# Kernel tuning notes

Measured on AMD Instinct MI355X. Metric: run time of the kernel, lower is better.

## Reference

```python
import jax, jax.numpy as jnp
import numpy as np

B, L, E, H = 64, 512, 128, 256
NEG_INF = -1e9  # finite stand-in for torch's -inf mask fill (same softmax result)


def setup_inputs() -> dict:
    key = jax.random.key(0)
    ks = jax.random.split(key, 12)
    s = 0.02
    return {
        "embed_input": jax.random.normal(ks[0], (B, L, E), jnp.float32),
        "decoder_input": jax.random.normal(ks[1], (B, E), jnp.float32),
        "h0": jax.random.normal(ks[2], (B, H), jnp.float32),
        "c0": jax.random.normal(ks[3], (B, H), jnp.float32),
        "context": jax.random.normal(ks[4], (B, L, H), jnp.float32),
        "Wih": jax.random.normal(ks[5], (E, 4 * H), jnp.float32) * s,
        "bih": jnp.zeros((4 * H,), jnp.float32),
        "Whh": jax.random.normal(ks[6], (H, 4 * H), jnp.float32) * s,
        "bhh": jnp.zeros((4 * H,), jnp.float32),
        "Wo": jax.random.normal(ks[7], (2 * H, H), jnp.float32) * s,
        "bo": jnp.zeros((H,), jnp.float32),
        "Wq": jax.random.normal(ks[8], (H, H), jnp.float32) * s,
        "bq": jnp.zeros((H,), jnp.float32),
        "Wc": jax.random.normal(ks[9], (H, H), jnp.float32) * s,
        "bc": jnp.zeros((H,), jnp.float32),
        "V": jax.random.uniform(ks[10], (H,), jnp.float32, minval=-1.0, maxval=1.0),
    }


def _forward(embed_input, decoder_input, h0, c0, context,
             Wih, bih, Whh, bhh, Wo, bo, Wq, bq, Wc, bc, V):
    Bq, Lq = embed_input.shape[0], embed_input.shape[1]
    # context_linear is a 1x1 conv -> loop-invariant linear; hoist out of the loop
    ctx = context @ Wc + bc  # (B, L, H)
    runner = jnp.arange(Lq)

    def step(carry, _):
        h, c, mask, x = carry
        # fused LSTM gates
        gates = x @ Wih + bih + h @ Whh + bhh  # (B, 4H)
        i_g, f_g, g_g, o_g = jnp.split(gates, 4, axis=1)
        c_t = jax.nn.sigmoid(f_g) * c + jax.nn.sigmoid(i_g) * jnp.tanh(g_g)
        h_t = jax.nn.sigmoid(o_g) * jnp.tanh(c_t)
        # pointer attention (additive, tanh, V-scored)
        q = h_t @ Wq + bq  # (B, H)
        att = jnp.einsum('h,blh->bl', V, jnp.tanh(q[:, None, :] + ctx))  # (B, L)
        att = jnp.where(mask == 0, NEG_INF, att)
        alpha = jax.nn.softmax(att, axis=1)  # (B, L)
        attn_h = jnp.einsum('bl,blh->bh', alpha, ctx)
        h_new = jnp.tanh(jnp.concatenate([attn_h, h_t], axis=1) @ Wo + bo)
        # masked argmax selection + gather of next decoder input
        masked = alpha * mask
        idx = jnp.argmax(masked, axis=1)  # (B,)
        one_hot = (runner[None, :] == idx[:, None]).astype(alpha.dtype)
        mask_new = mask * (1.0 - one_hot)
        x_new = jnp.einsum('bl,bld->bd', one_hot, embed_input)  # (B, E)
        return (h_new, c_t, mask_new, x_new), (alpha, idx)

    mask0 = jnp.ones((Bq, Lq), embed_input.dtype)
    (h_f, c_f, _, _), (alphas, idxs) = jax.lax.scan(
        step, (h0, c0, mask0, decoder_input), None, length=Lq)
    outputs = jnp.transpose(alphas, (1, 2, 0))  # (B, L, T) matching permute(1,2,0)
    pointers = jnp.transpose(idxs, (1, 0))      # (B, T)
    return outputs, pointers, h_f, c_f


def reference(embed_input, decoder_input, h0, c0, context,
              Wih, bih, Whh, bhh, Wo, bo, Wq, bq, Wc, bc, V):
    return _forward(embed_input, decoder_input, h0, c0, context,
                    Wih, bih, Whh, bhh, Wo, bo, Wq, bq, Wc, bc, V)
```

## Files before the change

### kernel.cpp

```cpp
#include <hip/hip_runtime.h>
#include <cstdint>
#include <cstddef>


#define DEV static __device__ __forceinline__

DEV float rl(float v, int l) {
    return __int_as_float(__builtin_amdgcn_readlane(__float_as_int(v), l));
}
DEV float fast_rcp(float d) {
    float r = __builtin_amdgcn_rcpf(d);
    return r * (2.0f - d * r);
}
DEV float fast_tanh(float x) {
    float e = __expf(fminf(2.0f * x, 88.0f));
    return 1.0f - 2.0f * fast_rcp(1.0f + e);
}
DEV float fast_sigmoid(float x) {
    float e = __expf(fminf(-x, 88.0f));
    return fast_rcp(1.0f + e);
}
DEV void st_rel_u32(uint32_t* p, uint32_t v) {
    __hip_atomic_store(p, v, __ATOMIC_RELEASE, __HIP_MEMORY_SCOPE_AGENT);
}
DEV uint32_t ld_acq_u32(const uint32_t* p) {
    return __hip_atomic_load(p, __ATOMIC_ACQUIRE, __HIP_MEMORY_SCOPE_AGENT);
}
DEV void st_f(float* p, float v) {
    __hip_atomic_store(p, v, __ATOMIC_RELAXED, __HIP_MEMORY_SCOPE_AGENT);
}
DEV float ld_f(const float* p) {
    return __hip_atomic_load(p, __ATOMIC_RELAXED, __HIP_MEMORY_SCOPE_AGENT);
}

__global__ __launch_bounds__(256) void k_ctx(const float* __restrict__ cin,
                                             const float* __restrict__ Wc,
                                             const float* __restrict__ bc,
                                             float* __restrict__ cout_) {
    __shared__ float rows[8][256];
    const int tid = threadIdx.x, lane = tid & 63;
    const long bl0 = (long)blockIdx.x * 8;
    for (int i = tid; i < 8 * 256; i += 256)
        rows[i >> 8][i & 255] = cin[bl0 * 256 + i];
    __syncthreads();
    float rr[8][4];
#pragma unroll
    for (int r = 0; r < 8; ++r)
#pragma unroll
        for (int q = 0; q < 4; ++q) rr[r][q] = rows[r][q * 64 + lane];
    float acc[8] = {0, 0, 0, 0, 0, 0, 0, 0};
#pragma unroll
    for (int kq = 0; kq < 4; ++kq) {
        for (int kk = 0; kk < 64; ++kk) {
            float wc = Wc[(kq * 64 + kk) * 256 + tid];
#pragma unroll
            for (int r = 0; r < 8; ++r) acc[r] += rl(rr[r][kq], kk) * wc;
        }
    }
    float bcv = bc[tid];
#pragma unroll
    for (int r = 0; r < 8; ++r) cout_[(bl0 + r) * 256 + tid] = acc[r] + bcv;
}

__global__ __launch_bounds__(256) void k_proj(const float* __restrict__ xin,
                                              const float* __restrict__ Wih,
                                              float* __restrict__ yout) {
    __shared__ float rows[8][128];
    const int tid = threadIdx.x, lane = tid & 63;
    const long bl0 = (long)blockIdx.x * 8;
    for (int i = tid; i < 8 * 128; i += 256)
        rows[i >> 7][i & 127] = xin[bl0 * 128 + i];
    __syncthreads();
    float rr[8][2];
#pragma unroll
    for (int r = 0; r < 8; ++r)
#pragma unroll
        for (int q = 0; q < 2; ++q) rr[r][q] = rows[r][q * 64 + lane];
    float4 acc[8];
#pragma unroll
    for (int r = 0; r < 8; ++r) acc[r] = make_float4(0.f, 0.f, 0.f, 0.f);
#pragma unroll
    for (int eq = 0; eq < 2; ++eq) {
        for (int ee = 0; ee < 64; ++ee) {
            const float4 w4 =
                *(const float4*)(Wih + (size_t)(eq * 64 + ee) * 1024 + tid * 4);
#pragma unroll
            for (int r = 0; r < 8; ++r) {
                float xe = rl(rr[r][eq], ee);
                acc[r].x += xe * w4.x; acc[r].y += xe * w4.y;
                acc[r].z += xe * w4.z; acc[r].w += xe * w4.w;
            }
        }
    }
#pragma unroll
    for (int r = 0; r < 8; ++r)
        *(float4*)(yout + (bl0 + r) * 1024 + tid * 4) = acc[r];
}

__global__ __launch_bounds__(256) void k_tr(const float* __restrict__ aws,
                                            float* __restrict__ out0) {
    __shared__ float tile[32][33];
    const int b = blockIdx.z, l0 = blockIdx.x * 32, t0 = blockIdx.y * 32;
    const int tx = threadIdx.x, ty = threadIdx.y;
    const float* src = aws + ((size_t)b << 18);
    float* dst = out0 + ((size_t)b << 18);
#pragma unroll
    for (int i = 0; i < 32; i += 8)
        tile[ty + i][tx] = src[(size_t)(t0 + ty + i) * 512 + l0 + tx];
    __syncthreads();
#pragma unroll
    for (int i = 0; i < 32; i += 8)
        dst[(size_t)(l0 + ty + i) * 512 + t0 + tx] = tile[tx][ty + i];
}

__global__ __launch_bounds__(1024) void k_zero(uint32_t* fl) {
    fl[threadIdx.x] = 0u;
    fl[1024 + threadIdx.x] = 0u;
}

__global__ __launch_bounds__(1024) void k_main4(
    const float* __restrict__ h0, const float* __restrict__ c0,
    const float* __restrict__ Whh, const float* __restrict__ Wq,
    const float* __restrict__ Wo, const float* __restrict__ bih,
    const float* __restrict__ bhh, const float* __restrict__ bq,
    const float* __restrict__ bo, const float* __restrict__ V,
    const float* __restrict__ ctx_ws, const float* __restrict__ emb_ws,
    const float* __restrict__ dec_ws, float* __restrict__ alpha_ws,
    float* __restrict__ out1, float* __restrict__ out2,
    float* __restrict__ out3, float* cg_ws, float* ca_ws, uint32_t* fl_ws) {
    const int g = blockIdx.x & 63;
    const int q = blockIdx.x >> 6;
    const int tid = threadIdx.x;
    const int lane = tid & 63;
    const int w = tid >> 6;

    __shared__ __align__(16) float h_s[256];
    __shared__ __align__(16) float c_s[256];
    __shared__ __align__(16) float q_s[256];
    __shared__ __align__(16) float ah_s[256];
    __shared__ __align__(16) float bsum_s[1024];
    __shared__ __align__(16) float att_s[512];
    __shared__ __align__(16) float alpha_s[512];
    __shared__ __align__(16) float mask_s[512];
    __shared__ __align__(16) float bq_s[256];
    __shared__ __align__(16) float bo_s[256];
    __shared__ __align__(16) float xp_s[1024];
    __shared__ __align__(16) float red_s[4096];
    __shared__ float wm_s[8], wS_s[8];
    __shared__ int wi_s[8];

    bsum_s[tid] = bih[tid] + bhh[tid];
    if (tid < 256) {
        h_s[tid] = h0[(g << 8) + tid];
        c_s[tid] = c0[(g << 8) + tid];
        bq_s[tid] = bq[tid];
        bo_s[tid] = bo[tid];
        *(float4*)(xp_s + (tid << 2)) =
            *(const float4*)(dec_ws + ((size_t)g << 10) + (tid << 2));
    }
    if (tid < 512) mask_s[tid] = 1.0f;
    const float4 V4 = *(const float4*)(V + (lane << 2));
    const float* cbase = ctx_ws + (((size_t)g << 9) << 8);
    __syncthreads();

    for (int t = 0; t < 512; ++t) {
        const int par = t & 1;
        const size_t gq4 = (size_t)(par * 64 + g) * 4;
        float* cgb = cg_ws + (gq4 << 10);
        float* cab = ca_ws + (gq4 << 7);
        uint32_t* fg = fl_ws + par * 256 + (g << 2);
        uint32_t* fa = fl_ws + 512 + par * 256 + (g << 2);

        if (tid < 256) {
            float hv = h_s[(q << 6) + lane];
            float4 acc = make_float4(0.f, 0.f, 0.f, 0.f);
            const float* wp = Whh + (size_t)(q << 6) * 1024 + (tid << 2);
#pragma unroll 16
            for (int kk = 0; kk < 64; ++kk) {
                float hk = rl(hv, kk);
                const float4 w4 = *(const float4*)(wp + (size_t)kk * 1024);
                acc.x += hk * w4.x; acc.y += hk * w4.y;
                acc.z += hk * w4.z; acc.w += hk * w4.w;
            }
            *(float4*)(red_s + (q << 10) + (tid << 2)) = acc;
        }
        __syncthreads();
        st_f(cgb + (q << 10) + tid, red_s[(q << 10) + tid]);
        __syncthreads();
        if (tid == 0) st_rel_u32(fg + q, (uint32_t)(t + 1));
        if (tid < 3) {
            const int pm = tid + (tid >= q ? 1 : 0);
            while (ld_acq_u32(fg + pm) < (uint32_t)(t + 1))
                __builtin_amdgcn_s_sleep(1);
        }
        __syncthreads();
#pragma unroll
        for (int jj = 0; jj < 4; ++jj)
            if (jj != q) red_s[(jj << 10) + tid] = ld_f(cgb + (jj << 10) + tid);
        __syncthreads();
        if (tid < 256) {
            float gi = red_s[tid] + red_s[1024 + tid] + red_s[2048 + tid] +
                       red_s[3072 + tid] + bsum_s[tid];
            float gf = red_s[256 + tid] + red_s[1280 + tid] +
                       red_s[2304 + tid] + red_s[3328 + tid] +
                       bsum_s[256 + tid];
            float gg = red_s[512 + tid] + red_s[1536 + tid] +
                       red_s[2560 + tid] + red_s[3584 + tid] +
                       bsum_s[512 + tid];
            float go = red_s[768 + tid] + red_s[1792 + tid] +
                       red_s[2816 + tid] + red_s[3840 + tid] +
                       bsum_s[768 + tid];
            gi += xp_s[tid]; gf += xp_s[256 + tid];
            gg += xp_s[512 + tid]; go += xp_s[768 + tid];
            float ig = fast_sigmoid(gi);
            float fg2 = fast_sigmoid(gf);
            float ggt = fast_tanh(gg);
            float og = fast_sigmoid(go);
            float cn = fg2 * c_s[tid] + ig * ggt;
            c_s[tid] = cn;
            h_s[tid] = og * fast_tanh(cn);
        }
        __syncthreads();
        if (tid < 256) {
            const int u = lane;
            const int pq = tid >> 6;
            float hv = h_s[(pq << 6) + u];
            float4 acc = make_float4(0.f, 0.f, 0.f, 0.f);
            const float* wp = Wq + (size_t)(pq << 6) * 256 + (u << 2);
#pragma unroll 8
            for (int kk = 0; kk < 64; ++kk) {
                float hk = rl(hv, kk);
                const float4 w4 = *(const float4*)(wp + (size_t)kk * 256);
                acc.x += hk * w4.x; acc.y += hk * w4.y;
                acc.z += hk * w4.z; acc.w += hk * w4.w;
            }
            *(float4*)(red_s + (pq << 8) + (u << 2)) = acc;
        }
        __syncthreads();
        if (tid < 256)
            q_s[tid] = red_s[tid] + red_s[256 + tid] + red_s[512 + tid] +
                       red_s[768 + tid] + bq_s[tid];
        __syncthreads();
        {
            const float4 q4 = *(const float4*)(q_s + (lane << 2));
#pragma unroll 2
            for (int i = 0; i < 8; ++i) {
                const int l = (q << 7) + (i << 4) + w;
                if (mask_s[l] == 0.f) {
                    if (lane == 0) att_s[l] = -1e9f;
                } else {
                    const float4 cc =
                        *(const float4*)(cbase + ((size_t)l << 8) + (lane << 2));
                    float s = V4.x * fast_tanh(q4.x + cc.x) +
                              V4.y * fast_tanh(q4.y + cc.y) +
                              V4.z * fast_tanh(q4.z + cc.z) +
                              V4.w * fast_tanh(q4.w + cc.w);
#pragma unroll
                    for (int off = 32; off > 0; off >>= 1)
                        s += __shfl_xor(s, off, 64);
                    if (lane == 0) att_s[l] = s;
                }
            }
        }
        __syncthreads();
        if (tid < 128) st_f(cab + (q << 7) + tid, att_s[(q << 7) + tid]);
        __syncthreads();
        if (tid == 0) st_rel_u32(fa + q, (uint32_t)(t + 1));
        if (tid < 3) {
            const int pm = tid + (tid >= q ? 1 : 0);
            while (ld_acq_u32(fa + pm) < (uint32_t)(t + 1))
                __builtin_amdgcn_s_sleep(1);
        }
        __syncthreads();
        if (tid < 384) {
            const int rel = tid >> 7;
            const int pm = rel + (rel >= q ? 1 : 0);
            const int word = tid & 127;
            att_s[(pm << 7) + word] = ld_f(cab + (pm << 7) + word);
        }
        __syncthreads();
        if (tid < 512) {
            float v = att_s[tid];
            int bi = tid;
#pragma unroll
            for (int off = 1; off < 64; off <<= 1) {
                float ov = __shfl_xor(v, off, 64);
                int oi = __shfl_xor(bi, off, 64);
                if (ov > v || (ov == v && oi < bi)) { v = ov; bi = oi; }
            }
            if (lane == 0) { wm_s[w] = v; wi_s[w] = bi; }
        }
        __syncthreads();
        float e_r = 0.f;
        float m_r; int idx_r;
        {
            m_r = wm_s[0]; idx_r = wi_s[0];
#pragma unroll
            for (int i = 1; i < 8; ++i) {
                float v2 = wm_s[i]; int i2 = wi_s[i];
                if (v2 > m_r || (v2 == m_r && i2 < idx_r)) { m_r = v2; idx_r = i2; }
            }
            if (tid < 512) {
                e_r = __expf(att_s[tid] - m_r);
                float ss = e_r;
#pragma unroll
                for (int off = 32; off > 0; off >>= 1)
                    ss += __shfl_xor(ss, off, 64);
                if (lane == 0) wS_s[w] = ss;
            }
        }
        __syncthreads();
        {
            float S = 0.f;
#pragma unroll
            for (int i = 0; i < 8; ++i) S += wS_s[i];
            if (tid < 512) {
                float a = e_r / S;
                alpha_s[tid] = a;
                if ((tid >> 7) == q)
                    alpha_ws[((((size_t)g << 9) + t) << 9) + tid] = a;
            }
            if (q == 0 && tid == 0) out1[(g << 9) + t] = (float)idx_r;
            if (tid == 0) mask_s[idx_r] = 0.f;
            if (tid < 256)
                *(float4*)(xp_s + (tid << 2)) = *(const float4*)(
                    emb_ws + ((size_t)((g << 9) + idx_r) << 10) + (tid << 2));
        }
        __syncthreads();
        {
            float ax = 0.f, ay = 0.f, az = 0.f, aw = 0.f;
            const float* cb2 = cbase + (lane << 2);
            for (int l = w; l < 512; l += 16) {
                float al = alpha_s[l];
                if (al != 0.f) {
                    const float4 cc = *(const float4*)(cb2 + ((size_t)l << 8));
                    ax += al * cc.x; ay += al * cc.y;
                    az += al * cc.z; aw += al * cc.w;
                }
            }
            *(float4*)(red_s + (w << 8) + (lane << 2)) =
                make_float4(ax, ay, az, aw);
        }
        __syncthreads();
        if (tid < 256) {
            float s = 0.f;
#pragma unroll
            for (int i = 0; i < 16; ++i) s += red_s[(i << 8) + tid];
            ah_s[tid] = s;
        }
        __syncthreads();
        if (tid < 256) {
            const int pq = tid >> 6;
            const float* src0 = (pq < 2) ? ah_s : h_s;
            float av0 = src0[((pq & 1) << 7) + lane];
            float av1 = src0[((pq & 1) << 7) + 64 + lane];
            const int c = (q << 6) + lane;
            float acc = 0.f;
            const float* wp = Wo + (size_t)(pq << 7) * 256 + c;
#pragma unroll 8
            for (int kk = 0; kk < 64; ++kk)
                acc += rl(av0, kk) * wp[(size_t)kk * 256];
#pragma unroll 8
            for (int kk = 0; kk < 64; ++kk)
                acc += rl(av1, kk) * wp[(size_t)(64 + kk) * 256];
            red_s[(pq << 6) + lane] = acc;
        }
        __syncthreads();
        if (tid < 64)
            h_s[(q << 6) + tid] =
                fast_tanh(red_s[tid] + red_s[64 + tid] + red_s[128 + tid] +
                          red_s[192 + tid] + bo_s[(q << 6) + tid]);
        __syncthreads();
    }
    if (tid < 64) out2[(g << 8) + (q << 6) + tid] = h_s[(q << 6) + tid];
    if (q == 0 && tid < 256) out3[(g << 8) + tid] = c_s[tid];
}

__global__ __launch_bounds__(1024) void k_main1(
    const float* __restrict__ h0, const float* __restrict__ c0,
    const float* __restrict__ Whh, const float* __restrict__ Wih,
    const float* __restrict__ Wq, const float* __restrict__ Wo,
    const float* __restrict__ bih, const float* __restrict__ bhh,
    const float* __restrict__ bq, const float* __restrict__ bo,
    const float* __restrict__ V, const float* __restrict__ embed,
    const float* __restrict__ dec_in, const float* __restrict__ ctx_ws,
    const float* __restrict__ emb_ws, const float* __restrict__ dec_ws,
    float* __restrict__ alpha_ws, float* __restrict__ out0,
    float* __restrict__ out1, float* __restrict__ out2,
    float* __restrict__ out3, int use_emb, int use_stage) {
    const int b = blockIdx.x;
    const int tid = threadIdx.x;
    const int lane = tid & 63;
    const int w = tid >> 6;
    const int tt = tid & 255;
    const int p = tid >> 8;

    __shared__ __align__(16) float h_s[256];
    __shared__ __align__(16) float c_s[256];
    __shared__ __align__(16) float q_s[256];
    __shared__ __align__(16) float ah_s[256];
    __shared__ __align__(16) float bsum_s[1024];
    __shared__ __align__(16) float att_s[512];
    __shared__ __align__(16) float alpha_s[512];
    __shared__ __align__(16) float mask_s[512];
    __shared__ __align__(16) float bq_s[256];
    __shared__ __align__(16) float bo_s[256];
    __shared__ __align__(16) float xp_s[1024];
    __shared__ __align__(16) float x_s[128];
    __shared__ __align__(16) float red_s[4096];
    __shared__ float wm_s[8], wS_s[8];
    __shared__ int wi_s[8];

    bsum_s[tid] = bih[tid] + bhh[tid];
    if (tid < 256) {
        h_s[tid] = h0[(b << 8) + tid];
        c_s[tid] = c0[(b << 8) + tid];
        bq_s[tid] = bq[tid];
        bo_s[tid] = bo[tid];
    }
    if (tid < 512) mask_s[tid] = 1.0f;
    if (use_emb) {
        if (tid < 256)
            *(float4*)(xp_s + (tid << 2)) =
                *(const float4*)(dec_ws + ((size_t)b << 10) + (tid << 2));
    } else {
        if (tid < 128) x_s[tid] = dec_in[(b << 7) + tid];
    }
    const float4 V4 = *(const float4*)(V + (lane << 2));
    const float* cbase = ctx_ws + (((size_t)b << 9) << 8);
    __syncthreads();

    for (int t = 0; t < 512; ++t) {
        {
            float hv = h_s[(p << 6) + lane];
            float4 acc = make_float4(0.f, 0.f, 0.f, 0.f);
            const float* wp = Whh + (size_t)(p << 6) * 1024 + (tt << 2);
#pragma unroll 16
            for (int kk = 0; kk < 64; ++kk) {
                float hk = rl(hv, kk);
                const float4 w4 = *(const float4*)(wp + (size_t)kk * 1024);
                acc.x += hk * w4.x; acc.y += hk * w4.y;
                acc.z += hk * w4.z; acc.w += hk * w4.w;
            }
            if (!use_emb) {
                float xv = x_s[(p << 5) + (lane & 31)];
                const float* wip = Wih + (size_t)(p << 5) * 1024 + (tt << 2);
#pragma unroll 8
                for (int ee = 0; ee < 32; ++ee) {
                    float xe = rl(xv, ee);
                    const float4 w4 = *(const float4*)(wip + (size_t)ee * 1024);
                    acc.x += xe * w4.x; acc.y += xe * w4.y;
                    acc.z += xe * w4.z; acc.w += xe * w4.w;
                }
            }
            *(float4*)(red_s + (p << 10) + (tt << 2)) = acc;
        }
        __syncthreads();
        if (tid < 256) {
            float gi = red_s[tid] + red_s[1024 + tid] + red_s[2048 + tid] +
                       red_s[3072 + tid] + bsum_s[tid];
            float gf = red_s[256 + tid] + red_s[1280 + tid] +
                       red_s[2304 + tid] + red_s[3328 + tid] +
                       bsum_s[256 + tid];
            float gg = red_s[512 + tid] + red_s[1536 + tid] +
                       red_s[2560 + tid] + red_s[3584 + tid] +
                       bsum_s[512 + tid];
            float go = red_s[768 + tid] + red_s[1792 + tid] +
                       red_s[2816 + tid] + red_s[3840 + tid] +
                       bsum_s[768 + tid];
            if (use_emb) {
                gi += xp_s[tid]; gf += xp_s[256 + tid];
                gg += xp_s[512 + tid]; go += xp_s[768 + tid];
            }
            float ig = fast_sigmoid(gi);
            float fg = fast_sigmoid(gf);
            float ggt = fast_tanh(gg);
            float og = fast_sigmoid(go);
            float cn = fg * c_s[tid] + ig * ggt;
            c_s[tid] = cn;
            h_s[tid] = og * fast_tanh(cn);
        }
        __syncthreads();
        if (tid < 256) {
            const int u = lane;
            const int pq = tid >> 6;
            float hv = h_s[(pq << 6) + u];
            float4 acc = make_float4(0.f, 0.f, 0.f, 0.f);
            const float* wp = Wq + (size_t)(pq << 6) * 256 + (u << 2);
#pragma unroll 8
            for (int kk = 0; kk < 64; ++kk) {
                float hk = rl(hv, kk);
                const float4 w4 = *(const float4*)(wp + (size_t)kk * 256);
                acc.x += hk * w4.x; acc.y += hk * w4.y;
                acc.z += hk * w4.z; acc.w += hk * w4.w;
            }
            *(float4*)(red_s + (pq << 8) + (u << 2)) = acc;
        }
        __syncthreads();
        if (tid < 256)
            q_s[tid] = red_s[tid] + red_s[256 + tid] + red_s[512 + tid] +
                       red_s[768 + tid] + bq_s[tid];
        __syncthreads();
        {
            const float4 q4 = *(const float4*)(q_s + (lane << 2));
#pragma unroll 2
            for (int l = w; l < 512; l += 16) {
                if (mask_s[l] == 0.f) {
                    if (lane == 0) att_s[l] = -1e9f;
                } else {
                    const float4 cc =
                        *(const float4*)(cbase + ((size_t)l << 8) + (lane << 2));
                    float s = V4.x * fast_tanh(q4.x + cc.x) +
                              V4.y * fast_tanh(q4.y + cc.y) +
                              V4.z * fast_tanh(q4.z + cc.z) +
                              V4.w * fast_tanh(q4.w + cc.w);
#pragma unroll
                    for (int off = 32; off > 0; off >>= 1)
                        s += __shfl_xor(s, off, 64);
                    if (lane == 0) att_s[l] = s;
                }
            }
        }
        __syncthreads();
        if (tid < 512) {
            float v = att_s[tid];
            int bi = tid;
#pragma unroll
            for (int off = 1; off < 64; off <<= 1) {
                float ov = __shfl_xor(v, off, 64);
                int oi = __shfl_xor(bi, off, 64);
                if (ov > v || (ov == v && oi < bi)) { v = ov; bi = oi; }
            }
            if (lane == 0) { wm_s[w] = v; wi_s[w] = bi; }
        }
        __syncthreads();
        float e_r = 0.f;
        float m_r; int idx_r;
        {
            m_r = wm_s[0]; idx_r = wi_s[0];
#pragma unroll
            for (int i = 1; i < 8; ++i) {
                float v2 = wm_s[i]; int i2 = wi_s[i];
                if (v2 > m_r || (v2 == m_r && i2 < idx_r)) { m_r = v2; idx_r = i2; }
            }
            if (tid < 512) {
                e_r = __expf(att_s[tid] - m_r);
                float ss = e_r;
#pragma unroll
                for (int off = 32; off > 0; off >>= 1)
                    ss += __shfl_xor(ss, off, 64);
                if (lane == 0) wS_s[w] = ss;
            }
        }
        __syncthreads();
        {
            float S = 0.f;
#pragma unroll
            for (int i = 0; i < 8; ++i) S += wS_s[i];
            if (tid < 512) {
                float a = e_r / S;
                alpha_s[tid] = a;
                if (use_stage)
                    alpha_ws[((((size_t)b << 9) + t) << 9) + tid] = a;
                else
                    out0[((size_t)b << 18) + ((size_t)tid << 9) + t] = a;
            }
            if (tid == 0) {
                out1[(b << 9) + t] = (float)idx_r;
                mask_s[idx_r] = 0.f;
            }
            if (use_emb) {
                if (tid < 256)
                    *(float4*)(xp_s + (tid << 2)) = *(const float4*)(
                        emb_ws + ((size_t)((b << 9) + idx_r) << 10) + (tid << 2));
            } else {
                if (tid < 128)
                    x_s[tid] = embed[((size_t)((b << 9) + idx_r) << 7) + tid];
            }
        }
        __syncthreads();
        {
            float ax = 0.f, ay = 0.f, az = 0.f, aw = 0.f;
            const float* cb2 = cbase + (lane << 2);
            for (int l = w; l < 512; l += 16) {
                float al = alpha_s[l];
                if (al != 0.f) {
                    const float4 cc = *(const float4*)(cb2 + ((size_t)l << 8));
                    ax += al * cc.x; ay += al * cc.y;
                    az += al * cc.z; aw += al * cc.w;
                }
            }
            *(float4*)(red_s + (w << 8) + (lane << 2)) =
                make_float4(ax, ay, az, aw);
        }
        __syncthreads();
        if (tid < 256) {
            float s = 0.f;
#pragma unroll
            for (int i = 0; i < 16; ++i) s += red_s[(i << 8) + tid];
            ah_s[tid] = s;
        }
        __syncthreads();
        if (tid < 256) {
            const int pq = tid >> 6, u = lane;
            const float* src0 = (pq < 2) ? ah_s : h_s;
            float av0 = src0[((pq & 1) << 7) + u];
            float av1 = src0[((pq & 1) << 7) + 64 + u];
            float4 acc = make_float4(0.f, 0.f, 0.f, 0.f);
            const float* wp = Wo + (size_t)(pq << 7) * 256 + (u << 2);
#pragma unroll 8
            for (int kk = 0; kk < 64; ++kk) {
                float hk = rl(av0, kk);
                const float4 w4 = *(const float4*)(wp + (size_t)kk * 256);
                acc.x += hk * w4.x; acc.y += hk * w4.y;
                acc.z += hk * w4.z; acc.w += hk * w4.w;
            }
#pragma unroll 8
            for (int kk = 0; kk < 64; ++kk) {
                float hk = rl(av1, kk);
                const float4 w4 = *(const float4*)(wp + (size_t)(64 + kk) * 256);
                acc.x += hk * w4.x; acc.y += hk * w4.y;
                acc.z += hk * w4.z; acc.w += hk * w4.w;
            }
            *(float4*)(red_s + (pq << 8) + (u << 2)) = acc;
        }
        __syncthreads();
        if (tid < 256)
            h_s[tid] = fast_tanh(red_s[tid] + red_s[256 + tid] +
                                 red_s[512 + tid] + red_s[768 + tid] + bo_s[tid]);
        __syncthreads();
    }
    if (tid < 256) {
        out2[(b << 8) + tid] = h_s[tid];
        out3[(b << 8) + tid] = c_s[tid];
    }
}

extern "C" void kernel_launch(void* const* d_in, const int* in_sizes, int n_in,
                              void* d_out, int out_size, void* d_ws,
                              size_t ws_size, hipStream_t stream) {
    const float* embed = (const float*)d_in[0];
    const float* dec   = (const float*)d_in[1];
    const float* h0    = (const float*)d_in[2];
    const float* c0    = (const float*)d_in[3];
    const float* ctxin = (const float*)d_in[4];
    const float* Wih   = (const float*)d_in[5];
    const float* bih   = (const float*)d_in[6];
    const float* Whh   = (const float*)d_in[7];
    const float* bhh   = (const float*)d_in[8];
    const float* Wo    = (const float*)d_in[9];
    const float* bo    = (const float*)d_in[10];
    const float* Wq    = (const float*)d_in[11];
    const float* bq    = (const float*)d_in[12];
    const float* Wc    = (const float*)d_in[13];
    const float* bc    = (const float*)d_in[14];
    const float* V     = (const float*)d_in[15];

    float* out0 = (float*)d_out;
    float* out1 = out0 + 16777216;
    float* out2 = out1 + 32768;
    float* out3 = out2 + 16384;

    float* ws = (float*)d_ws;
    const size_t wsf = ws_size / 4;
    const size_t SZ_CTX = 8388608, SZ_DEC = 65536, SZ_EMB = 33554432,
                 SZ_AL = 16777216;
    const size_t SZ_CG = 2ull * 64 * 4 * 1024;
    const size_t SZ_CA = 2ull * 64 * 4 * 128;
    const size_t SZ_FL = 4096;
    const int use_emb = wsf >= SZ_CTX + SZ_DEC + SZ_EMB;
    const size_t al_off = use_emb ? (SZ_CTX + SZ_DEC + SZ_EMB) : SZ_CTX;
    const int use_stage = wsf >= al_off + SZ_AL;
    const size_t comm_off = al_off + SZ_AL;
    const int use_split =
        use_emb && use_stage && (wsf >= comm_off + SZ_CG + SZ_CA + SZ_FL);

    float* ws_ctx = ws;
    float* ws_dec = ws + SZ_CTX;
    float* ws_emb = ws + SZ_CTX + SZ_DEC;
    float* ws_al  = ws + al_off;
    float* ws_cg  = ws + comm_off;
    float* ws_ca  = ws_cg + SZ_CG;
    uint32_t* ws_fl = (uint32_t*)(ws_ca + SZ_CA);

    k_ctx<<<dim3(4096), dim3(256), 0, stream>>>(ctxin, Wc, bc, ws_ctx);
    if (use_emb) {
        k_proj<<<dim3(4096), dim3(256), 0, stream>>>(embed, Wih, ws_emb);
        k_proj<<<dim3(8), dim3(256), 0, stream>>>(dec, Wih, ws_dec);
    }
    if (use_split) {
        k_zero<<<dim3(1), dim3(1024), 0, stream>>>(ws_fl);
        k_main4<<<dim3(256), dim3(1024), 0, stream>>>(
            h0, c0, Whh, Wq, Wo, bih, bhh, bq, bo, V, ws_ctx, ws_emb, ws_dec,
            ws_al, out1, out2, out3, ws_cg, ws_ca, ws_fl);
    } else {
        k_main1<<<dim3(64), dim3(1024), 0, stream>>>(
            h0, c0, Whh, Wih, Wq, Wo, bih, bhh, bq, bo, V, embed, dec, ws_ctx,
            ws_emb, ws_dec, ws_al, out0, out1, out2, out3, use_emb, use_stage);
    }
    if (use_stage)
        k_tr<<<dim3(16, 16, 64), dim3(32, 8), 0, stream>>>(ws_al, out0);
}
```

Baseline: 15.58 ms.

## Keep Whh slice in registers, spread matvecs over all threads, trim barriers

Each thread now caches its 64-element column of the Whh slice in registers once before the time loop, instead of re-reading Whh from global memory every step. The recurrent and Wq matvecs are spread over all 1024 threads with scalar accumulators rather than 256 threads using float4. Partial gate sums from peer blocks are read straight from global memory into registers, and attention scores are written to global as they are produced, which removes several __syncthreads. The 64 extra registers per thread may raise register pressure or cause spills, and the Wq loads become scalar.

```diff
diff --git a/kernel.cpp b/kernel.cpp
--- a/kernel.cpp
+++ b/kernel.cpp
@@ -149,6 +149,13 @@
     __shared__ float wm_s[8], wS_s[8];
     __shared__ int wi_s[8];
 
+    float whh_r[64];
+    {
+        const float* wp = Whh + (size_t)(q << 6) * 1024 + tid;
+#pragma unroll
+        for (int kk = 0; kk < 64; ++kk) whh_r[kk] = wp[(size_t)kk * 1024];
+    }
+
     bsum_s[tid] = bih[tid] + bhh[tid];
     if (tid < 256) {
         h_s[tid] = h0[(g << 8) + tid];
@@ -171,21 +178,14 @@
         uint32_t* fg = fl_ws + par * 256 + (g << 2);
         uint32_t* fa = fl_ws + 512 + par * 256 + (g << 2);
 
-        if (tid < 256) {
+        {
             float hv = h_s[(q << 6) + lane];
-            float4 acc = make_float4(0.f, 0.f, 0.f, 0.f);
-            const float* wp = Whh + (size_t)(q << 6) * 1024 + (tid << 2);
-#pragma unroll 16
-            for (int kk = 0; kk < 64; ++kk) {
-                float hk = rl(hv, kk);
-                const float4 w4 = *(const float4*)(wp + (size_t)kk * 1024);
-                acc.x += hk * w4.x; acc.y += hk * w4.y;
-                acc.z += hk * w4.z; acc.w += hk * w4.w;
-            }
-            *(float4*)(red_s + (q << 10) + (tid << 2)) = acc;
-        }
-        __syncthreads();
-        st_f(cgb + (q << 10) + tid, red_s[(q << 10) + tid]);
+            float acc = 0.f;
+#pragma unroll
+            for (int kk = 0; kk < 64; ++kk) acc += rl(hv, kk) * whh_r[kk];
+            red_s[(q << 10) + tid] = acc;
+            st_f(cgb + (q << 10) + tid, acc);
+        }
         __syncthreads();
         if (tid == 0) st_rel_u32(fg + q, (uint32_t)(t + 1));
         if (tid < 3) {
@@ -194,21 +194,23 @@
                 __builtin_amdgcn_s_sleep(1);
         }
         __syncthreads();
-#pragma unroll
-        for (int jj = 0; jj < 4; ++jj)
-            if (jj != q) red_s[(jj << 10) + tid] = ld_f(cgb + (jj << 10) + tid);
-        __syncthreads();
         if (tid < 256) {
-            float gi = red_s[tid] + red_s[1024 + tid] + red_s[2048 + tid] +
-                       red_s[3072 + tid] + bsum_s[tid];
-            float gf = red_s[256 + tid] + red_s[1280 + tid] +
-                       red_s[2304 + tid] + red_s[3328 + tid] +
+            float pj[4][4];
+#pragma unroll
+            for (int j = 0; j < 4; ++j) {
+#pragma unroll
+                for (int o = 0; o < 4; ++o) {
+                    pj[j][o] = (j == q)
+                                   ? red_s[(j << 10) + (o << 8) + tid]
+                                   : ld_f(cgb + (j << 10) + (o << 8) + tid);
+                }
+            }
+            float gi = pj[0][0] + pj[1][0] + pj[2][0] + pj[3][0] + bsum_s[tid];
+            float gf = pj[0][1] + pj[1][1] + pj[2][1] + pj[3][1] +
                        bsum_s[256 + tid];
-            float gg = red_s[512 + tid] + red_s[1536 + tid] +
-                       red_s[2560 + tid] + red_s[3584 + tid] +
+            float gg = pj[0][2] + pj[1][2] + pj[2][2] + pj[3][2] +
                        bsum_s[512 + tid];
-            float go = red_s[768 + tid] + red_s[1792 + tid] +
-                       red_s[2816 + tid] + red_s[3840 + tid] +
+            float go = pj[0][3] + pj[1][3] + pj[2][3] + pj[3][3] +
                        bsum_s[768 + tid];
             gi += xp_s[tid]; gf += xp_s[256 + tid];
             gg += xp_s[512 + tid]; go += xp_s[768 + tid];
@@ -221,20 +223,16 @@
             h_s[tid] = og * fast_tanh(cn);
         }
         __syncthreads();
-        if (tid < 256) {
-            const int u = lane;
-            const int pq = tid >> 6;
-            float hv = h_s[(pq << 6) + u];
-            float4 acc = make_float4(0.f, 0.f, 0.f, 0.f);
-            const float* wp = Wq + (size_t)(pq << 6) * 256 + (u << 2);
+        {
+            const int pq = tid >> 8;
+            const int c = tid & 255;
+            float hv = h_s[(pq << 6) + lane];
+            float acc = 0.f;
+            const float* wp = Wq + (size_t)(pq << 6) * 256 + c;
 #pragma unroll 8
-            for (int kk = 0; kk < 64; ++kk) {
-                float hk = rl(hv, kk);
-                const float4 w4 = *(const float4*)(wp + (size_t)kk * 256);
-                acc.x += hk * w4.x; acc.y += hk * w4.y;
-                acc.z += hk * w4.z; acc.w += hk * w4.w;
-            }
-            *(float4*)(red_s + (pq << 8) + (u << 2)) = acc;
+            for (int kk = 0; kk < 64; ++kk)
+                acc += rl(hv, kk) * wp[(size_t)kk * 256];
+            red_s[(pq << 8) + c] = acc;
         }
         __syncthreads();
         if (tid < 256)
@@ -247,7 +245,7 @@
             for (int i = 0; i < 8; ++i) {
                 const int l = (q << 7) + (i << 4) + w;
                 if (mask_s[l] == 0.f) {
-                    if (lane == 0) att_s[l] = -1e9f;
+                    if (lane == 0) { att_s[l] = -1e9f; st_f(cab + l, -1e9f); }
                 } else {
                     const float4 cc =
                         *(const float4*)(cbase + ((size_t)l << 8) + (lane << 2));
@@ -258,12 +256,10 @@
 #pragma unroll
                     for (int off = 32; off > 0; off >>= 1)
                         s += __shfl_xor(s, off, 64);
-                    if (lane == 0) att_s[l] = s;
+                    if (lane == 0) { att_s[l] = s; st_f(cab + l, s); }
                 }
             }
         }
-        __syncthreads();
-        if (tid < 128) st_f(cab + (q << 7) + tid, att_s[(q << 7) + tid]);
         __syncthreads();
         if (tid == 0) st_rel_u32(fa + q, (uint32_t)(t + 1));
         if (tid < 3) {
```

New measurement: 27.52 ms. 1.77x slower.
